# Optimization experiments

Measured on AMD Instinct MI355X. Metric: run time of the kernel, lower is better.

Reference implementation:

```python
import jax, jax.numpy as jnp
import numpy as np

B, S, D = 4, 2048, 1024
DFF = 4 * D
NE = 4        # routed experts
NS = 2        # shared experts
TOPK = 2
CAP_F = 1.25


def _gelu(v):
    return jax.nn.gelu(v, approximate=False)  # torch nn.GELU default (erf)


def setup_inputs() -> dict:
    key = jax.random.key(0)
    ks = jax.random.split(key, 9)
    s = 0.02
    f = lambda k, sh: jax.random.normal(k, sh, dtype=jnp.float32) * s
    return {
        "hidden_states": jax.random.normal(ks[0], (B, S, D), dtype=jnp.float32),
        "router_w1": f(ks[1], (D, D)), "router_b1": jnp.zeros((D,), jnp.float32),
        "router_w2": f(ks[2], (D, NE)), "router_b2": jnp.zeros((NE,), jnp.float32),
        "re_w1": f(ks[3], (NE, D, DFF)), "re_b1": jnp.zeros((NE, DFF), jnp.float32),
        "re_w2": f(ks[4], (NE, DFF, D)), "re_b2": jnp.zeros((NE, D), jnp.float32),
        "se_w1": f(ks[5], (NS, D, DFF)), "se_b1": jnp.zeros((NS, DFF), jnp.float32),
        "se_w2": f(ks[6], (NS, DFF, D)), "se_b2": jnp.zeros((NS, D), jnp.float32),
        "out_w": f(ks[7], (D, D)), "out_b": jnp.zeros((D,), jnp.float32),
    }


def reference(hidden_states, router_w1, router_b1, router_w2, router_b2,
              re_w1, re_b1, re_w2, re_b2, se_w1, se_b1, se_w2, se_b2,
              out_w, out_b):
    b, s, d = hidden_states.shape
    T = b * s
    x = hidden_states.reshape(T, d)

    # --- router ---
    logits = _gelu(x @ router_w1 + router_b1) @ router_w2 + router_b2  # [T, NE]
    top_v, top_i = jax.lax.top_k(logits, TOPK)
    rweights = jax.nn.softmax(top_v, axis=-1)                          # [T, TOPK]
    z_loss = jnp.mean(jnp.square(jax.nn.logsumexp(logits, axis=-1)))

    capacity = int(T / NE * CAP_F)  # static Python int

    # padded token slot T absorbs dropped/overflow contributions, discarded later
    x_pad = jnp.concatenate([x, jnp.zeros((1, d), x.dtype)], axis=0)
    final = jnp.zeros((T + 1, d), x.dtype)

    for i in range(TOPK):
        eidx = top_i[:, i]
        w_pad = jnp.concatenate([rweights[:, i], jnp.zeros((1,), x.dtype)])
        for j in range(NE):
            # first `capacity` tokens routed to expert j (deterministic capacity drop)
            idx = jnp.nonzero(eidx == j, size=capacity, fill_value=T)[0]  # [capacity]
            h = _gelu(x_pad[idx] @ re_w1[j] + re_b1[j]) @ re_w2[j] + re_b2[j]
            final = final.at[idx].add(w_pad[idx][:, None] * h)
    final = final[:T]

    # shared experts (dense, weight 1/NS each)
    for j in range(NS):
        final = final + (1.0 / NS) * (_gelu(x @ se_w1[j] + se_b1[j]) @ se_w2[j] + se_b2[j])

    out = final @ out_w + out_b
    out = out * 0.5 + x * 0.5
    mu = jnp.mean(out, axis=-1, keepdims=True)
    var = jnp.var(out, axis=-1, keepdims=True)
    out = (out - mu) / jnp.sqrt(var + 1e-6)  # layer_norm, no affine, eps=1e-6
    return out.reshape(b, s, d), z_loss
```

## Files before the change

kernel.cpp:

```cpp
#include <hip/hip_runtime.h>
#include <hip/hip_bf16.h>
#include <math.h>

#define TTOK 8192
#define DM 1024
#define DFFN 4096
#define NEXP 4
#define CAPACITY 2560
#define EROWSN (2*CAPACITY)

typedef short bf16x8 __attribute__((ext_vector_type(8)));
typedef float f32x4 __attribute__((ext_vector_type(4)));

__device__ __forceinline__ unsigned short f2bf(float f) {
  unsigned int u = __float_as_uint(f);
  u = (u + 0x7fffu + ((u >> 16) & 1u)) >> 16;
  return (unsigned short)u;
}
__device__ __forceinline__ float bf2f(unsigned short h) {
  return __uint_as_float(((unsigned int)h) << 16);
}
__device__ __forceinline__ float gelu_f(float v) {
  float z = fabsf(v) * 0.7071067811865476f;
  float t = 1.0f / (1.0f + 0.3275911f * z);
  float p = t * (0.254829592f +
            t * (-0.284496736f +
            t * (1.421413741f +
            t * (-1.453152027f + t * 1.061405429f))));
  float er = 1.0f - p * __expf(-z * z);
  er = v >= 0.f ? er : -er;
  return 0.5f * v * (1.0f + er);
}
__device__ __forceinline__ void gl16(const void* g, void* l) {
  __builtin_amdgcn_global_load_lds((const __attribute__((address_space(1))) void*)g,
                                   (__attribute__((address_space(3))) void*)l, 16, 0, 0);
}

__global__ void k_cvt_x(const float* __restrict__ x, unsigned short* __restrict__ xhi,
                        unsigned short* __restrict__ xlo) {
  int i = blockIdx.x * blockDim.x + threadIdx.x;
  const int n4 = (TTOK + 1) * DM / 4;
  if (i >= n4) return;
  int base = i * 4;
  float v[4] = {0.f, 0.f, 0.f, 0.f};
  if (base < TTOK * DM) {
    float4 f = *reinterpret_cast<const float4*>(x + base);
    v[0] = f.x; v[1] = f.y; v[2] = f.z; v[3] = f.w;
  }
  ushort4 h, l;
  unsigned short hh[4], ll[4];
#pragma unroll
  for (int j = 0; j < 4; j++) {
    hh[j] = f2bf(v[j]);
    ll[j] = f2bf(v[j] - bf2f(hh[j]));
  }
  h.x = hh[0]; h.y = hh[1]; h.z = hh[2]; h.w = hh[3];
  l.x = ll[0]; l.y = ll[1]; l.z = ll[2]; l.w = ll[3];
  reinterpret_cast<ushort4*>(xhi)[i] = h;
  reinterpret_cast<ushort4*>(xlo)[i] = l;
}

__global__ void k_tcvt(const float* __restrict__ W, unsigned short* __restrict__ Wt,
                       int K, int N) {
  __shared__ float tile[32][33];
  int tx = threadIdx.x, ty = threadIdx.y;
  int n0 = blockIdx.x * 32, k0 = blockIdx.y * 32;
#pragma unroll
  for (int i = 0; i < 4; i++)
    tile[ty + i * 8][tx] = W[(size_t)(k0 + ty + i * 8) * N + n0 + tx];
  __syncthreads();
#pragma unroll
  for (int i = 0; i < 4; i++)
    Wt[(size_t)(n0 + ty + i * 8) * K + k0 + tx] = f2bf(tile[tx][ty + i * 8]);
}

__global__ void k_tcvt2(const float* __restrict__ W, unsigned short* __restrict__ Whi,
                        unsigned short* __restrict__ Wlo, int K, int N) {
  __shared__ float tile[32][33];
  int tx = threadIdx.x, ty = threadIdx.y;
  int n0 = blockIdx.x * 32, k0 = blockIdx.y * 32;
#pragma unroll
  for (int i = 0; i < 4; i++)
    tile[ty + i * 8][tx] = W[(size_t)(k0 + ty + i * 8) * N + n0 + tx];
  __syncthreads();
#pragma unroll
  for (int i = 0; i < 4; i++) {
    float v = tile[tx][ty + i * 8];
    unsigned short h = f2bf(v);
    Whi[(size_t)(n0 + ty + i * 8) * K + k0 + tx] = h;
    Wlo[(size_t)(n0 + ty + i * 8) * K + k0 + tx] = f2bf(v - bf2f(h));
  }
}

__global__ __launch_bounds__(256) void k_router(
    const unsigned short* __restrict__ xhi, const unsigned short* __restrict__ xlo,
    const unsigned short* __restrict__ whi, const unsigned short* __restrict__ wlo,
    const float* __restrict__ bias, float* __restrict__ Hr) {
  const int t = threadIdx.x;
  const int m0 = blockIdx.y * 128, n0 = blockIdx.x * 128;
  __shared__ unsigned short sAh[2][4096], sAl[2][4096], sBh[2][4096], sBl[2][4096];
  const int offA0 = t * 16, offA1 = offA0 + 4096;
  const int i0 = offA0 >> 1, i1 = offA1 >> 1;
  const int r0 = offA0 >> 6, c0e = (offA0 & 63) >> 1;
  const int r1 = offA1 >> 6, c1e = (offA1 & 63) >> 1;
  const unsigned short* pAh0 = xhi + (size_t)(m0 + r0) * DM + c0e;
  const unsigned short* pAh1 = xhi + (size_t)(m0 + r1) * DM + c1e;
  const unsigned short* pAl0 = xlo + (size_t)(m0 + r0) * DM + c0e;
  const unsigned short* pAl1 = xlo + (size_t)(m0 + r1) * DM + c1e;
  const unsigned short* pBh0 = whi + (size_t)(n0 + r0) * DM + c0e;
  const unsigned short* pBh1 = whi + (size_t)(n0 + r1) * DM + c1e;
  const unsigned short* pBl0 = wlo + (size_t)(n0 + r0) * DM + c0e;
  const unsigned short* pBl1 = wlo + (size_t)(n0 + r1) * DM + c1e;
  const int lane = t & 63, wid = t >> 6;
  const int wm = (wid >> 1) * 64, wn = (wid & 1) * 64;
  const int fr = lane & 15, fk = (lane >> 4) * 8;
  f32x4 acc[4][4];
#pragma unroll
  for (int m = 0; m < 4; m++)
#pragma unroll
    for (int n = 0; n < 4; n++) acc[m][n] = (f32x4){0.f, 0.f, 0.f, 0.f};

  auto stage = [&](int b, int k) {
    gl16(pAh0 + k, &sAh[b][i0]); gl16(pAh1 + k, &sAh[b][i1]);
    gl16(pAl0 + k, &sAl[b][i0]); gl16(pAl1 + k, &sAl[b][i1]);
    gl16(pBh0 + k, &sBh[b][i0]); gl16(pBh1 + k, &sBh[b][i1]);
    gl16(pBl0 + k, &sBl[b][i0]); gl16(pBl1 + k, &sBl[b][i1]);
  };

  int cur = 0;
  stage(0, 0);
  __syncthreads();
  for (int k0 = 0; k0 < DM; k0 += 32) {
    if (k0 + 32 < DM) stage(cur ^ 1, k0 + 32);
    bf16x8 ah[4], al[4], bh[4], bl[4];
#pragma unroll
    for (int m = 0; m < 4; m++) {
      ah[m] = *reinterpret_cast<const bf16x8*>(&sAh[cur][(wm + m * 16 + fr) * 32 + fk]);
      al[m] = *reinterpret_cast<const bf16x8*>(&sAl[cur][(wm + m * 16 + fr) * 32 + fk]);
    }
#pragma unroll
    for (int n = 0; n < 4; n++) {
      bh[n] = *reinterpret_cast<const bf16x8*>(&sBh[cur][(wn + n * 16 + fr) * 32 + fk]);
      bl[n] = *reinterpret_cast<const bf16x8*>(&sBl[cur][(wn + n * 16 + fr) * 32 + fk]);
    }
#pragma unroll
    for (int m = 0; m < 4; m++)
#pragma unroll
      for (int n = 0; n < 4; n++) {
        acc[m][n] = __builtin_amdgcn_mfma_f32_16x16x32_bf16(ah[m], bh[n], acc[m][n], 0, 0, 0);
        acc[m][n] = __builtin_amdgcn_mfma_f32_16x16x32_bf16(ah[m], bl[n], acc[m][n], 0, 0, 0);
        acc[m][n] = __builtin_amdgcn_mfma_f32_16x16x32_bf16(al[m], bh[n], acc[m][n], 0, 0, 0);
      }
    __syncthreads();
    cur ^= 1;
  }
  const int er = (lane >> 4) * 4, ec = lane & 15;
#pragma unroll
  for (int n = 0; n < 4; n++) {
    const int cc = n0 + wn + n * 16 + ec;
    const float bn = bias[cc];
#pragma unroll
    for (int m = 0; m < 4; m++) {
      const int rbase = m0 + wm + m * 16 + er;
#pragma unroll
      for (int j = 0; j < 4; j++)
        Hr[(size_t)(rbase + j) * DM + cc] = gelu_f(acc[m][n][j] + bn);
    }
  }
}

template <int MODE>
__global__ __launch_bounds__(256) void k_gemm(
    const unsigned short* __restrict__ A, const unsigned short* __restrict__ Bt,
    const float* __restrict__ bias, float* __restrict__ outF,
    unsigned short* __restrict__ outBf, const int* __restrict__ rows,
    const float* __restrict__ rwgt, const int* __restrict__ rowsPad, int N, int K) {
  if constexpr (MODE == 0 || MODE == 2) {
    if ((int)(blockIdx.y * 128) >= rowsPad[0]) return;
  }
  const int t = threadIdx.x;
  const int m0 = blockIdx.y * 128, n0 = blockIdx.x * 128;
  int kbeg = 0, klen = K;
  if constexpr (MODE == 2) { kbeg = blockIdx.z * (K >> 1); klen = K >> 1; }
  __shared__ unsigned short smem[16384];
  const int offA0 = t * 16, offA1 = offA0 + 4096;
  const int i0 = offA0 >> 1, i1 = offA1 >> 1;
  const int r0 = offA0 >> 6, c0e = (offA0 & 63) >> 1;
  const int r1 = offA1 >> 6, c1e = (offA1 & 63) >> 1;
  size_t ar0 = m0 + r0, ar1 = m0 + r1;
  if constexpr (MODE == 0) { ar0 = rows[ar0]; ar1 = rows[ar1]; }
  const unsigned short* pA0 = A + ar0 * (size_t)K + kbeg + c0e;
  const unsigned short* pA1 = A + ar1 * (size_t)K + kbeg + c1e;
  const unsigned short* pB0 = Bt + (size_t)(n0 + r0) * K + kbeg + c0e;
  const unsigned short* pB1 = Bt + (size_t)(n0 + r1) * K + kbeg + c1e;
  const int lane = t & 63, wid = t >> 6;
  const int wm = (wid >> 1) * 64, wn = (wid & 1) * 64;
  const int fr = lane & 15, fk = (lane >> 4) * 8;
  f32x4 acc[4][4];
#pragma unroll
  for (int m = 0; m < 4; m++)
#pragma unroll
    for (int n = 0; n < 4; n++) acc[m][n] = (f32x4){0.f, 0.f, 0.f, 0.f};

  auto stage = [&](int b, int k) {
    gl16(pA0 + k, smem + b * 4096 + i0); gl16(pA1 + k, smem + b * 4096 + i1);
    gl16(pB0 + k, smem + 8192 + b * 4096 + i0); gl16(pB1 + k, smem + 8192 + b * 4096 + i1);
  };

  int cur = 0;
  stage(0, 0);
  __syncthreads();
  for (int k0 = 0; k0 < klen; k0 += 32) {
    if (k0 + 32 < klen) stage(cur ^ 1, k0 + 32);
    bf16x8 av[4], bv[4];
#pragma unroll
    for (int m = 0; m < 4; m++)
      av[m] = *reinterpret_cast<const bf16x8*>(smem + cur * 4096 + (wm + m * 16 + fr) * 32 + fk);
#pragma unroll
    for (int n = 0; n < 4; n++)
      bv[n] = *reinterpret_cast<const bf16x8*>(smem + 8192 + cur * 4096 + (wn + n * 16 + fr) * 32 + fk);
#pragma unroll
    for (int m = 0; m < 4; m++)
#pragma unroll
      for (int n = 0; n < 4; n++)
        acc[m][n] = __builtin_amdgcn_mfma_f32_16x16x32_bf16(av[m], bv[n], acc[m][n], 0, 0, 0);
    __syncthreads();
    cur ^= 1;
  }
  const int er = (lane >> 4) * 4, ec = lane & 15;
  if constexpr (MODE <= 1) {
    unsigned short* cb = smem + wid * 4096;
#pragma unroll
    for (int n = 0; n < 4; n++) {
      const int cc = n0 + wn + n * 16 + ec;
      const float bn = bias[cc];
#pragma unroll
      for (int m = 0; m < 4; m++) {
#pragma unroll
        for (int j = 0; j < 4; j++) {
          int row = m * 16 + er + j;
          int col = n * 16 + ec;
          int addr = row * 64 + ((((col >> 3) ^ (row & 7)) << 3) | (col & 7));
          cb[addr] = f2bf(gelu_f(acc[m][n][j] + bn));
        }
      }
    }
#pragma unroll
    for (int it = 0; it < 8; it++) {
      int row = it * 8 + (lane >> 3);
      int cblk = lane & 7;
      int laddr = row * 64 + ((cblk ^ (row & 7)) << 3);
      bf16x8 v = *reinterpret_cast<const bf16x8*>(cb + laddr);
      *reinterpret_cast<bf16x8*>(outBf + (size_t)(m0 + wm + row) * N + (n0 + wn) + cblk * 8) = v;
    }
  } else {
#pragma unroll
    for (int n = 0; n < 4; n++) {
      const int cc = n0 + wn + n * 16 + ec;
      const float bn = bias[cc];
#pragma unroll
      for (int m = 0; m < 4; m++) {
        const int rbase = m0 + wm + m * 16 + er;
#pragma unroll
        for (int j = 0; j < 4; j++) {
          const int rr = rbase + j;
          if constexpr (MODE == 2) {
            float v = acc[m][n][j] + (blockIdx.z == 0 ? bn : 0.f);
            const int tok = rows[rr];
            if (tok < TTOK) atomicAdd(outF + (size_t)tok * DM + cc, rwgt[rr] * v);
          } else if constexpr (MODE == 3) {
            float* p = outF + (size_t)rr * DM + cc;
            *p += 0.5f * (acc[m][n][j] + bn);
          } else {
            outF[(size_t)rr * N + cc] = acc[m][n][j] + bn;
          }
        }
      }
    }
  }
}

__global__ __launch_bounds__(256) void k_logits(const float* __restrict__ Hr,
                                                const float* __restrict__ w2,
                                                const float* __restrict__ b2,
                                                float* __restrict__ logits) {
  int tok = blockIdx.x * 4 + (threadIdx.x >> 6);
  int lane = threadIdx.x & 63;
  const float* h = Hr + (size_t)tok * DM;
  float s0 = 0.f, s1 = 0.f, s2 = 0.f, s3 = 0.f;
  for (int d = lane; d < DM; d += 64) {
    float hv = h[d];
    s0 += hv * w2[d * 4 + 0];
    s1 += hv * w2[d * 4 + 1];
    s2 += hv * w2[d * 4 + 2];
    s3 += hv * w2[d * 4 + 3];
  }
#pragma unroll
  for (int off = 32; off >= 1; off >>= 1) {
    s0 += __shfl_down(s0, off, 64);
    s1 += __shfl_down(s1, off, 64);
    s2 += __shfl_down(s2, off, 64);
    s3 += __shfl_down(s3, off, 64);
  }
  if (lane == 0) {
    logits[tok * 4 + 0] = s0 + b2[0];
    logits[tok * 4 + 1] = s1 + b2[1];
    logits[tok * 4 + 2] = s2 + b2[2];
    logits[tok * 4 + 3] = s3 + b2[3];
  }
}

__global__ void k_topk(const float* __restrict__ logits, int* __restrict__ e0,
                       int* __restrict__ e1, float* __restrict__ w0,
                       float* __restrict__ w1, float* __restrict__ zout) {
  int tok = blockIdx.x * blockDim.x + threadIdx.x;
  if (tok >= TTOK) return;
  float l[4];
#pragma unroll
  for (int j = 0; j < 4; j++) l[j] = logits[tok * 4 + j];
  int i0 = 0; float v0 = l[0];
#pragma unroll
  for (int j = 1; j < 4; j++) if (l[j] > v0) { v0 = l[j]; i0 = j; }
  int i1 = -1; float v1 = -1e30f;
#pragma unroll
  for (int j = 0; j < 4; j++) if (j != i0 && l[j] > v1) { v1 = l[j]; i1 = j; }
  float d = expf(v1 - v0);
  float a = 1.f / (1.f + d);
  e0[tok] = i0; e1[tok] = i1;
  w0[tok] = a;  w1[tok] = d * a;
  float se = 0.f;
#pragma unroll
  for (int j = 0; j < 4; j++) se += expf(l[j] - v0);
  float lse = v0 + logf(se);
  atomicAdd(zout, lse * lse * (1.0f / TTOK));
}

__global__ __launch_bounds__(256) void k_lists(const int* __restrict__ e0,
                                               const int* __restrict__ e1,
                                               const float* __restrict__ w0,
                                               const float* __restrict__ w1,
                                               int* __restrict__ list,
                                               float* __restrict__ lwgt,
                                               int* __restrict__ cnt) {
  int b = blockIdx.x;
  int prio = b >> 2, j = b & 3;
  const int* e = prio ? e1 : e0;
  const float* w = prio ? w1 : w0;
  __shared__ int warpsum[4];
  __shared__ int sbase;
  if (threadIdx.x == 0) sbase = 0;
  __syncthreads();
  int lane = threadIdx.x & 63, wv = threadIdx.x >> 6;
  for (int t0 = 0; t0 < TTOK; t0 += 256) {
    int tok = t0 + threadIdx.x;
    bool p = (e[tok] == j);
    unsigned long long bal = __ballot(p);
    int pre = __popcll(bal & ((1ull << lane) - 1ull));
    if (lane == 0) warpsum[wv] = __popcll(bal);
    __syncthreads();
    int woff = 0;
    for (int q = 0; q < wv; q++) woff += warpsum[q];
    int tot = warpsum[0] + warpsum[1] + warpsum[2] + warpsum[3];
    int slot = sbase + woff + pre;
    if (p && slot < CAPACITY) {
      list[b * CAPACITY + slot] = tok;
      lwgt[b * CAPACITY + slot] = w[tok];
    }
    __syncthreads();
    if (threadIdx.x == 0) sbase += tot;
    __syncthreads();
  }
  if (threadIdx.x == 0) cnt[b] = min(sbase, CAPACITY);
}

__global__ void k_combine(const int* __restrict__ list, const float* __restrict__ lwgt,
                          const int* __restrict__ cnt, int* __restrict__ erows,
                          float* __restrict__ ewgt, int* __restrict__ rowsPad) {
  int j = blockIdx.x;
  int c0 = cnt[j], c1 = cnt[4 + j];
  for (int s = threadIdx.x; s < EROWSN; s += blockDim.x) {
    int tok = TTOK; float wv = 0.f;
    if (s < c0) { tok = list[j * CAPACITY + s]; wv = lwgt[j * CAPACITY + s]; }
    else if (s < c0 + c1) {
      tok = list[(4 + j) * CAPACITY + (s - c0)];
      wv = lwgt[(4 + j) * CAPACITY + (s - c0)];
    }
    erows[j * EROWSN + s] = tok;
    ewgt[j * EROWSN + s] = wv;
  }
  if (threadIdx.x == 0) rowsPad[j] = ((c0 + c1 + 127) / 128) * 128;
}

__global__ void k_cvt_final(const float* __restrict__ f, unsigned short* __restrict__ fb) {
  int i = blockIdx.x * blockDim.x + threadIdx.x;
  if (i >= TTOK * DM / 4) return;
  float4 v = reinterpret_cast<const float4*>(f)[i];
  ushort4 o;
  o.x = f2bf(v.x); o.y = f2bf(v.y); o.z = f2bf(v.z); o.w = f2bf(v.w);
  reinterpret_cast<ushort4*>(fb)[i] = o;
}

__global__ __launch_bounds__(256) void k_ln(const float* __restrict__ OUT,
                                            const float* __restrict__ x,
                                            float* __restrict__ out) {
  int r = blockIdx.x;
  const float* o = OUT + (size_t)r * DM;
  const float* xr = x + (size_t)r * DM;
  int t = threadIdx.x;
  float v[4];
  float s = 0.f, s2 = 0.f;
#pragma unroll
  for (int i = 0; i < 4; i++) {
    int d = t + i * 256;
    float val = 0.5f * o[d] + 0.5f * xr[d];
    v[i] = val; s += val; s2 += val * val;
  }
#pragma unroll
  for (int off = 32; off >= 1; off >>= 1) {
    s += __shfl_down(s, off, 64);
    s2 += __shfl_down(s2, off, 64);
  }
  __shared__ float rs[4], rs2[4];
  int wv = t >> 6, lane = t & 63;
  if (lane == 0) { rs[wv] = s; rs2[wv] = s2; }
  __syncthreads();
  s = rs[0] + rs[1] + rs[2] + rs[3];
  s2 = rs2[0] + rs2[1] + rs2[2] + rs2[3];
  float mu = s * (1.f / DM);
  float var = s2 * (1.f / DM) - mu * mu;
  float inv = 1.0f / sqrtf(var + 1e-6f);
#pragma unroll
  for (int i = 0; i < 4; i++)
    out[(size_t)r * DM + t + i * 256] = (v[i] - mu) * inv;
}

static constexpr size_t OFF_XHI = 0;
static constexpr size_t SZ_XHI = (size_t)(TTOK + 1) * DM * 2;
static constexpr size_t OFF_ACT = OFF_XHI + SZ_XHI;
static constexpr size_t SZ_ACT = (size_t)TTOK * DFFN * 2;
static constexpr size_t OFF_WBUF = OFF_ACT + SZ_ACT;
static constexpr size_t SZ_WBUF = (size_t)2 * DM * DFFN * 2;
static constexpr size_t OFF_FINAL = OFF_WBUF + SZ_WBUF;
static constexpr size_t SZ_FINAL = (size_t)TTOK * DM * 4;
static constexpr size_t OFF_MISC = OFF_FINAL + SZ_FINAL;
static constexpr size_t OFF_LOGITS = OFF_MISC;
static constexpr size_t OFF_E0 = OFF_LOGITS + (size_t)TTOK * 4 * 4;
static constexpr size_t OFF_E1 = OFF_E0 + (size_t)TTOK * 4;
static constexpr size_t OFF_W0 = OFF_E1 + (size_t)TTOK * 4;
static constexpr size_t OFF_W1 = OFF_W0 + (size_t)TTOK * 4;
static constexpr size_t OFF_LIST = OFF_W1 + (size_t)TTOK * 4;
static constexpr size_t OFF_LWGT = OFF_LIST + (size_t)8 * CAPACITY * 4;
static constexpr size_t OFF_CNT = OFF_LWGT + (size_t)8 * CAPACITY * 4;
static constexpr size_t OFF_EROWS = OFF_CNT + 64;
static constexpr size_t OFF_EWGT = OFF_EROWS + (size_t)NEXP * EROWSN * 4;
static constexpr size_t OFF_RPAD = OFF_EWGT + (size_t)NEXP * EROWSN * 4;

extern "C" void kernel_launch(void* const* d_in, const int* in_sizes, int n_in,
                              void* d_out, int out_size, void* d_ws, size_t ws_size,
                              hipStream_t stream) {
  const float* x = (const float*)d_in[0];
  const float* rw1 = (const float*)d_in[1];
  const float* rb1 = (const float*)d_in[2];
  const float* rw2 = (const float*)d_in[3];
  const float* rb2 = (const float*)d_in[4];
  const float* re_w1 = (const float*)d_in[5];
  const float* re_b1 = (const float*)d_in[6];
  const float* re_w2 = (const float*)d_in[7];
  const float* re_b2 = (const float*)d_in[8];
  const float* se_w1 = (const float*)d_in[9];
  const float* se_b1 = (const float*)d_in[10];
  const float* se_w2 = (const float*)d_in[11];
  const float* se_b2 = (const float*)d_in[12];
  const float* out_w = (const float*)d_in[13];
  const float* out_b = (const float*)d_in[14];
  float* outp = (float*)d_out;

  char* ws = (char*)d_ws;
  unsigned short* xhi = (unsigned short*)(ws + OFF_XHI);
  float* Hr = (float*)(ws + OFF_ACT);
  unsigned short* xlo = (unsigned short*)(ws + OFF_ACT + 33554432);
  unsigned short* act = (unsigned short*)(ws + OFF_ACT);
  unsigned short* fbf = (unsigned short*)(ws + OFF_ACT);
  float* OUTb = (float*)(ws + OFF_ACT + 16777216);
  unsigned short* w1t = (unsigned short*)(ws + OFF_WBUF);
  unsigned short* w2t = w1t + (size_t)DM * DFFN;
  unsigned short* rwhi = w1t;
  unsigned short* rwlo = w1t + (size_t)DM * DM;
  unsigned short* owt = w1t;
  float* finalb = (float*)(ws + OFF_FINAL);
  float* logits = (float*)(ws + OFF_LOGITS);
  int* e0 = (int*)(ws + OFF_E0);
  int* e1 = (int*)(ws + OFF_E1);
  float* w0 = (float*)(ws + OFF_W0);
  float* w1 = (float*)(ws + OFF_W1);
  int* list = (int*)(ws + OFF_LIST);
  float* lwgt = (float*)(ws + OFF_LWGT);
  int* cnt = (int*)(ws + OFF_CNT);
  int* erows = (int*)(ws + OFF_EROWS);
  float* ewgt = (float*)(ws + OFF_EWGT);
  int* rpad = (int*)(ws + OFF_RPAD);
  float* zout = outp + (size_t)TTOK * DM;

  hipMemsetAsync(finalb, 0, SZ_FINAL, stream);
  hipMemsetAsync(zout, 0, 4, stream);

  {
    int n4 = (TTOK + 1) * DM / 4;
    k_cvt_x<<<(n4 + 255) / 256, 256, 0, stream>>>(x, xhi, xlo);
  }
  k_tcvt2<<<dim3(DM / 32, DM / 32), dim3(32, 8), 0, stream>>>(rw1, rwhi, rwlo, DM, DM);
  k_router<<<dim3(DM / 128, TTOK / 128), 256, 0, stream>>>(xhi, xlo, rwhi, rwlo, rb1, Hr);
  k_logits<<<TTOK / 4, 256, 0, stream>>>(Hr, rw2, rb2, logits);
  k_topk<<<TTOK / 256, 256, 0, stream>>>(logits, e0, e1, w0, w1, zout);
  k_lists<<<8, 256, 0, stream>>>(e0, e1, w0, w1, list, lwgt, cnt);
  k_combine<<<NEXP, 256, 0, stream>>>(list, lwgt, cnt, erows, ewgt, rpad);

  for (int j = 0; j < NEXP; j++) {
    k_tcvt<<<dim3(DFFN / 32, DM / 32), dim3(32, 8), 0, stream>>>(
        re_w1 + (size_t)j * DM * DFFN, w1t, DM, DFFN);
    k_tcvt<<<dim3(DM / 32, DFFN / 32), dim3(32, 8), 0, stream>>>(
        re_w2 + (size_t)j * DFFN * DM, w2t, DFFN, DM);
    k_gemm<0><<<dim3(DFFN / 128, EROWSN / 128), 256, 0, stream>>>(
        xhi, w1t, re_b1 + (size_t)j * DFFN, nullptr, act,
        erows + (size_t)j * EROWSN, nullptr, rpad + j, DFFN, DM);
    k_gemm<2><<<dim3(DM / 128, EROWSN / 128, 2), 256, 0, stream>>>(
        act, w2t, re_b2 + (size_t)j * DM, finalb, nullptr,
        erows + (size_t)j * EROWSN, ewgt + (size_t)j * EROWSN, rpad + j, DM, DFFN);
  }
  for (int j = 0; j < 2; j++) {
    k_tcvt<<<dim3(DFFN / 32, DM / 32), dim3(32, 8), 0, stream>>>(
        se_w1 + (size_t)j * DM * DFFN, w1t, DM, DFFN);
    k_tcvt<<<dim3(DM / 32, DFFN / 32), dim3(32, 8), 0, stream>>>(
        se_w2 + (size_t)j * DFFN * DM, w2t, DFFN, DM);
    k_gemm<1><<<dim3(DFFN / 128, TTOK / 128), 256, 0, stream>>>(
        xhi, w1t, se_b1 + (size_t)j * DFFN, nullptr, act, nullptr, nullptr, nullptr,
        DFFN, DM);
    k_gemm<3><<<dim3(DM / 128, TTOK / 128), 256, 0, stream>>>(
        act, w2t, se_b2 + (size_t)j * DM, finalb, nullptr, nullptr, nullptr, nullptr,
        DM, DFFN);
  }
  k_cvt_final<<<TTOK * DM / 4 / 256, 256, 0, stream>>>(finalb, fbf);
  k_tcvt<<<dim3(DM / 32, DM / 32), dim3(32, 8), 0, stream>>>(out_w, owt, DM, DM);
  k_gemm<4><<<dim3(DM / 128, TTOK / 128), 256, 0, stream>>>(
      fbf, owt, out_b, OUTb, nullptr, nullptr, nullptr, nullptr, DM, DM);
  k_ln<<<TTOK, 256, 0, stream>>>(OUTb, x, outp);
}
```

Baseline: 1.210 ms.

## Replace 128x128 GEMM with 256x256 tiled, 8-wave pipelined kernel with split-K

```diff
diff --git a/kernel.cpp b/kernel.cpp
--- a/kernel.cpp
+++ b/kernel.cpp
@@ -170,110 +170,179 @@
 }
 
 template <int MODE>
-__global__ __launch_bounds__(256) void k_gemm(
+__global__ __launch_bounds__(512, 2) void k_gemm256(
     const unsigned short* __restrict__ A, const unsigned short* __restrict__ Bt,
     const float* __restrict__ bias, float* __restrict__ outF,
     unsigned short* __restrict__ outBf, const int* __restrict__ rows,
-    const float* __restrict__ rwgt, const int* __restrict__ rowsPad, int N, int K) {
+    const float* __restrict__ rwgt, const int* __restrict__ rowsPad,
+    int N, int K, int klen) {
   if constexpr (MODE == 0 || MODE == 2) {
-    if ((int)(blockIdx.y * 128) >= rowsPad[0]) return;
-  }
-  const int t = threadIdx.x;
-  const int m0 = blockIdx.y * 128, n0 = blockIdx.x * 128;
-  int kbeg = 0, klen = K;
-  if constexpr (MODE == 2) { kbeg = blockIdx.z * (K >> 1); klen = K >> 1; }
-  __shared__ unsigned short smem[16384];
-  const int offA0 = t * 16, offA1 = offA0 + 4096;
-  const int i0 = offA0 >> 1, i1 = offA1 >> 1;
-  const int r0 = offA0 >> 6, c0e = (offA0 & 63) >> 1;
-  const int r1 = offA1 >> 6, c1e = (offA1 & 63) >> 1;
-  size_t ar0 = m0 + r0, ar1 = m0 + r1;
-  if constexpr (MODE == 0) { ar0 = rows[ar0]; ar1 = rows[ar1]; }
-  const unsigned short* pA0 = A + ar0 * (size_t)K + kbeg + c0e;
-  const unsigned short* pA1 = A + ar1 * (size_t)K + kbeg + c1e;
-  const unsigned short* pB0 = Bt + (size_t)(n0 + r0) * K + kbeg + c0e;
-  const unsigned short* pB1 = Bt + (size_t)(n0 + r1) * K + kbeg + c1e;
-  const int lane = t & 63, wid = t >> 6;
-  const int wm = (wid >> 1) * 64, wn = (wid & 1) * 64;
-  const int fr = lane & 15, fk = (lane >> 4) * 8;
-  f32x4 acc[4][4];
-#pragma unroll
-  for (int m = 0; m < 4; m++)
-#pragma unroll
-    for (int n = 0; n < 4; n++) acc[m][n] = (f32x4){0.f, 0.f, 0.f, 0.f};
-
-  auto stage = [&](int b, int k) {
-    gl16(pA0 + k, smem + b * 4096 + i0); gl16(pA1 + k, smem + b * 4096 + i1);
-    gl16(pB0 + k, smem + 8192 + b * 4096 + i0); gl16(pB1 + k, smem + 8192 + b * 4096 + i1);
+    if ((int)(blockIdx.y * 256) >= rowsPad[0]) return;
+  }
+  __shared__ unsigned short lds[65536];
+  const int tid = threadIdx.x;
+  const int lane = tid & 63, wid = tid >> 6;
+  const int wr = wid >> 2, wc = wid & 3;
+  const int fr = lane & 15, fkb = (lane >> 4) * 16;
+  const int m0 = blockIdx.y * 256, n0 = blockIdx.x * 256;
+  int kbeg = 0;
+  if constexpr (MODE == 2 || MODE == 3) kbeg = blockIdx.z * klen;
+  const int nt = klen >> 6;
+  const int niter = nt >> 1;
+
+  const unsigned short *srcA[2][2], *srcB[2][2];
+#pragma unroll
+  for (int h = 0; h < 2; h++)
+#pragma unroll
+    for (int r = 0; r < 2; r++) {
+      int o = h * 16384 + r * 8192 + tid * 16;
+      int L = o ^ (((o >> 9) & 1) << 5);
+      int row = L >> 7, k = (L & 127) >> 1;
+      size_t arow;
+      if constexpr (MODE == 0) arow = (size_t)rows[m0 + row];
+      else arow = (size_t)(m0 + row);
+      srcA[h][r] = A + arow * (size_t)K + kbeg + k;
+      srcB[h][r] = Bt + (size_t)(n0 + row) * K + kbeg + k;
+    }
+  auto stA = [&](int buf, int h, int t) {
+    unsigned short* d = lds + buf * 16384 + h * 8192 + tid * 8;
+    gl16(srcA[h][0] + t * 64, d);
+    gl16(srcA[h][1] + t * 64, d + 4096);
   };
-
-  int cur = 0;
-  stage(0, 0);
-  __syncthreads();
-  for (int k0 = 0; k0 < klen; k0 += 32) {
-    if (k0 + 32 < klen) stage(cur ^ 1, k0 + 32);
-    bf16x8 av[4], bv[4];
-#pragma unroll
-    for (int m = 0; m < 4; m++)
-      av[m] = *reinterpret_cast<const bf16x8*>(smem + cur * 4096 + (wm + m * 16 + fr) * 32 + fk);
-#pragma unroll
-    for (int n = 0; n < 4; n++)
-      bv[n] = *reinterpret_cast<const bf16x8*>(smem + 8192 + cur * 4096 + (wn + n * 16 + fr) * 32 + fk);
-#pragma unroll
-    for (int m = 0; m < 4; m++)
-#pragma unroll
-      for (int n = 0; n < 4; n++)
-        acc[m][n] = __builtin_amdgcn_mfma_f32_16x16x32_bf16(av[m], bv[n], acc[m][n], 0, 0, 0);
-    __syncthreads();
-    cur ^= 1;
-  }
+  auto stB = [&](int buf, int h, int t) {
+    unsigned short* d = lds + 32768 + buf * 16384 + h * 8192 + tid * 8;
+    gl16(srcB[h][0] + t * 64, d);
+    gl16(srcB[h][1] + t * 64, d + 4096);
+  };
+
+  f32x4 acc[8][4];
+#pragma unroll
+  for (int a = 0; a < 8; a++)
+#pragma unroll
+    for (int b = 0; b < 4; b++) acc[a][b] = (f32x4){0.f, 0.f, 0.f, 0.f};
+
+  const int sw = ((fr >> 2) & 1) << 5;
+  const int aoff_s = fr * 64 + ((fkb ^ sw) >> 1);
+
+  stA(0, 0, 0); stB(0, 0, 0); stA(0, 1, 0); stB(0, 1, 0);
+  stA(1, 0, 1); stB(1, 0, 1);
+  asm volatile("s_waitcnt vmcnt(4)" ::: "memory");
+  __builtin_amdgcn_s_barrier();
+  __builtin_amdgcn_sched_barrier(0);
+
+  for (int i = 0; i < niter; ++i) {
+    const int t0 = 2 * i;
+    const bool last = (i == niter - 1);
+#pragma unroll
+    for (int q = 0; q < 8; ++q) {
+      const int buf = q >> 2, mh = (q >> 1) & 1, nh = q & 1;
+      bf16x8 af[4][2], bfr[2][2];
+      const unsigned short* Ab = lds + buf * 16384 + mh * 8192 + wr * 4096 + aoff_s;
+      const unsigned short* Bb = lds + 32768 + buf * 16384 + nh * 8192 + wc * 2048 + aoff_s;
+#pragma unroll
+      for (int m = 0; m < 4; m++)
+#pragma unroll
+        for (int kk = 0; kk < 2; kk++)
+          af[m][kk] = *reinterpret_cast<const bf16x8*>(Ab + m * 1024 + kk * 32);
+#pragma unroll
+      for (int n = 0; n < 2; n++)
+#pragma unroll
+        for (int kk = 0; kk < 2; kk++)
+          bfr[n][kk] = *reinterpret_cast<const bf16x8*>(Bb + n * 1024 + kk * 32);
+      if (q == 0)      stA(1, 1, t0 + 1);
+      else if (q == 1) stB(1, 1, t0 + 1);
+      else if (q == 2) { if (!last) stA(0, 0, t0 + 2); }
+      else if (q == 3) { if (!last) stB(0, 0, t0 + 2); }
+      else if (q == 4) { if (!last) stA(0, 1, t0 + 2); }
+      else if (q == 5) { if (!last) stB(0, 1, t0 + 2); }
+      else if (q == 6) { if (t0 + 3 < nt) stA(1, 0, t0 + 3); }
+      else             { if (t0 + 3 < nt) stB(1, 0, t0 + 3); }
+      if (q == 3) {
+        if (last) { asm volatile("s_waitcnt vmcnt(0)" ::: "memory"); }
+        else      { asm volatile("s_waitcnt vmcnt(4)" ::: "memory"); }
+      } else if (q == 7 && !last) {
+        asm volatile("s_waitcnt vmcnt(4)" ::: "memory");
+      }
+      __builtin_amdgcn_sched_barrier(0);
+      __builtin_amdgcn_s_barrier();
+      asm volatile("s_waitcnt lgkmcnt(0)" ::: "memory");
+      __builtin_amdgcn_sched_barrier(0);
+      __builtin_amdgcn_s_setprio(1);
+#pragma unroll
+      for (int m = 0; m < 4; m++)
+#pragma unroll
+        for (int n = 0; n < 2; n++)
+#pragma unroll
+          for (int kk = 0; kk < 2; kk++)
+            acc[mh * 4 + m][nh * 2 + n] = __builtin_amdgcn_mfma_f32_16x16x32_bf16(
+                af[m][kk], bfr[n][kk], acc[mh * 4 + m][nh * 2 + n], 0, 0, 0);
+      __builtin_amdgcn_s_setprio(0);
+      __builtin_amdgcn_sched_barrier(0);
+      __builtin_amdgcn_s_barrier();
+      __builtin_amdgcn_sched_barrier(0);
+    }
+  }
+
   const int er = (lane >> 4) * 4, ec = lane & 15;
   if constexpr (MODE <= 1) {
-    unsigned short* cb = smem + wid * 4096;
-#pragma unroll
-    for (int n = 0; n < 4; n++) {
-      const int cc = n0 + wn + n * 16 + ec;
+    unsigned short* cb = lds + wid * 8192;
+#pragma unroll
+    for (int b = 0; b < 4; b++) {
+      const int nh = b >> 1, n = b & 1;
+      const int cc = n0 + nh * 128 + wc * 32 + n * 16 + ec;
       const float bn = bias[cc];
-#pragma unroll
-      for (int m = 0; m < 4; m++) {
+      const int cl = nh * 32 + n * 16 + ec;
+#pragma unroll
+      for (int a = 0; a < 8; a++) {
+        const int mh = a >> 2, m = a & 3;
 #pragma unroll
         for (int j = 0; j < 4; j++) {
-          int row = m * 16 + er + j;
-          int col = n * 16 + ec;
-          int addr = row * 64 + ((((col >> 3) ^ (row & 7)) << 3) | (col & 7));
-          cb[addr] = f2bf(gelu_f(acc[m][n][j] + bn));
+          int rl = mh * 64 + m * 16 + er + j;
+          int addr = rl * 64 + ((((cl >> 3) ^ (rl & 7)) << 3) | (cl & 7));
+          cb[addr] = f2bf(gelu_f(acc[a][b][j] + bn));
         }
       }
     }
 #pragma unroll
-    for (int it = 0; it < 8; it++) {
-      int row = it * 8 + (lane >> 3);
+    for (int it = 0; it < 16; it++) {
+      int rl = it * 8 + (lane >> 3);
       int cblk = lane & 7;
-      int laddr = row * 64 + ((cblk ^ (row & 7)) << 3);
+      int laddr = rl * 64 + ((cblk ^ (rl & 7)) << 3);
       bf16x8 v = *reinterpret_cast<const bf16x8*>(cb + laddr);
-      *reinterpret_cast<bf16x8*>(outBf + (size_t)(m0 + wm + row) * N + (n0 + wn) + cblk * 8) = v;
+      int grow = m0 + (rl >> 6) * 128 + wr * 64 + (rl & 63);
+      int gcol = n0 + (cblk >> 2) * 128 + wc * 32 + (cblk & 3) * 8;
+      *reinterpret_cast<bf16x8*>(outBf + (size_t)grow * N + gcol) = v;
     }
   } else {
-#pragma unroll
-    for (int n = 0; n < 4; n++) {
-      const int cc = n0 + wn + n * 16 + ec;
-      const float bn = bias[cc];
-#pragma unroll
-      for (int m = 0; m < 4; m++) {
-        const int rbase = m0 + wm + m * 16 + er;
-#pragma unroll
-        for (int j = 0; j < 4; j++) {
-          const int rr = rbase + j;
-          if constexpr (MODE == 2) {
-            float v = acc[m][n][j] + (blockIdx.z == 0 ? bn : 0.f);
-            const int tok = rows[rr];
-            if (tok < TTOK) atomicAdd(outF + (size_t)tok * DM + cc, rwgt[rr] * v);
-          } else if constexpr (MODE == 3) {
-            float* p = outF + (size_t)rr * DM + cc;
-            *p += 0.5f * (acc[m][n][j] + bn);
-          } else {
-            outF[(size_t)rr * N + cc] = acc[m][n][j] + bn;
+    float bnz[4];
+    int ccs[4];
+#pragma unroll
+    for (int b = 0; b < 4; b++) {
+      ccs[b] = n0 + (b >> 1) * 128 + wc * 32 + (b & 1) * 16 + ec;
+      if constexpr (MODE == 4) bnz[b] = bias[ccs[b]];
+      else bnz[b] = (blockIdx.z == 0) ? bias[ccs[b]] : 0.f;
+    }
+#pragma unroll
+    for (int a = 0; a < 8; a++) {
+#pragma unroll
+      for (int j = 0; j < 4; j++) {
+        const int rr = m0 + (a >> 2) * 128 + wr * 64 + (a & 3) * 16 + er + j;
+        if constexpr (MODE == 2) {
+          const int tok = rows[rr];
+          if (tok < TTOK) {
+            const float w = rwgt[rr];
+#pragma unroll
+            for (int b = 0; b < 4; b++)
+              atomicAdd(outF + (size_t)tok * DM + ccs[b], w * (acc[a][b][j] + bnz[b]));
           }
+        } else if constexpr (MODE == 3) {
+#pragma unroll
+          for (int b = 0; b < 4; b++)
+            atomicAdd(outF + (size_t)rr * DM + ccs[b], 0.5f * (acc[a][b][j] + bnz[b]));
+        } else {
+#pragma unroll
+          for (int b = 0; b < 4; b++)
+            outF[(size_t)rr * N + ccs[b]] = acc[a][b][j] + bnz[b];
         }
       }
     }
@@ -388,7 +457,7 @@
     erows[j * EROWSN + s] = tok;
     ewgt[j * EROWSN + s] = wv;
   }
-  if (threadIdx.x == 0) rowsPad[j] = ((c0 + c1 + 127) / 128) * 128;
+  if (threadIdx.x == 0) rowsPad[j] = ((c0 + c1 + 255) / 256) * 256;
 }
 
 __global__ void k_cvt_final(const float* __restrict__ f, unsigned short* __restrict__ fb) {
@@ -520,28 +589,28 @@
         re_w1 + (size_t)j * DM * DFFN, w1t, DM, DFFN);
     k_tcvt<<<dim3(DM / 32, DFFN / 32), dim3(32, 8), 0, stream>>>(
         re_w2 + (size_t)j * DFFN * DM, w2t, DFFN, DM);
-    k_gemm<0><<<dim3(DFFN / 128, EROWSN / 128), 256, 0, stream>>>(
+    k_gemm256<0><<<dim3(DFFN / 256, EROWSN / 256), 512, 0, stream>>>(
         xhi, w1t, re_b1 + (size_t)j * DFFN, nullptr, act,
-        erows + (size_t)j * EROWSN, nullptr, rpad + j, DFFN, DM);
-    k_gemm<2><<<dim3(DM / 128, EROWSN / 128, 2), 256, 0, stream>>>(
+        erows + (size_t)j * EROWSN, nullptr, rpad + j, DFFN, DM, DM);
+    k_gemm256<2><<<dim3(DM / 256, EROWSN / 256, 4), 512, 0, stream>>>(
         act, w2t, re_b2 + (size_t)j * DM, finalb, nullptr,
-        erows + (size_t)j * EROWSN, ewgt + (size_t)j * EROWSN, rpad + j, DM, DFFN);
+        erows + (size_t)j * EROWSN, ewgt + (size_t)j * EROWSN, rpad + j, DM, DFFN, 1024);
   }
   for (int j = 0; j < 2; j++) {
     k_tcvt<<<dim3(DFFN / 32, DM / 32), dim3(32, 8), 0, stream>>>(
         se_w1 + (size_t)j * DM * DFFN, w1t, DM, DFFN);
     k_tcvt<<<dim3(DM / 32, DFFN / 32), dim3(32, 8), 0, stream>>>(
         se_w2 + (size_t)j * DFFN * DM, w2t, DFFN, DM);
-    k_gemm<1><<<dim3(DFFN / 128, TTOK / 128), 256, 0, stream>>>(
+    k_gemm256<1><<<dim3(DFFN / 256, TTOK / 256), 512, 0, stream>>>(
         xhi, w1t, se_b1 + (size_t)j * DFFN, nullptr, act, nullptr, nullptr, nullptr,
-        DFFN, DM);
-    k_gemm<3><<<dim3(DM / 128, TTOK / 128), 256, 0, stream>>>(
+        DFFN, DM, DM);
+    k_gemm256<3><<<dim3(DM / 256, TTOK / 256, 2), 512, 0, stream>>>(
         act, w2t, se_b2 + (size_t)j * DM, finalb, nullptr, nullptr, nullptr, nullptr,
-        DM, DFFN);
+        DM, DFFN, 2048);
   }
   k_cvt_final<<<TTOK * DM / 4 / 256, 256, 0, stream>>>(finalb, fbf);
   k_tcvt<<<dim3(DM / 32, DM / 32), dim3(32, 8), 0, stream>>>(out_w, owt, DM, DM);
-  k_gemm<4><<<dim3(DM / 128, TTOK / 128), 256, 0, stream>>>(
-      fbf, owt, out_b, OUTb, nullptr, nullptr, nullptr, nullptr, DM, DM);
+  k_gemm256<4><<<dim3(DM / 256, TTOK / 256), 512, 0, stream>>>(
+      fbf, owt, out_b, OUTb, nullptr, nullptr, nullptr, nullptr, DM, DM, DM);
   k_ln<<<TTOK, 256, 0, stream>>>(OUTb, x, outp);
 }
```

After: 1.538 ms. +27.1%, slower.
